# Optimization experiments

Hardware: AMD Instinct MI355X
Metric: run time of the kernel (lower is better)

Reference implementation:

```python
import jax, jax.numpy as jnp
import numpy as np
import math

D_MODEL = 768
NUM_HEADS = 12
HEAD_DIM = D_MODEL // NUM_HEADS
HIDDEN = 3072
EPS = 1e-05
CLAMP = 1e9


def setup_inputs() -> dict:
    key = jax.random.key(0)
    ks = jax.random.split(key, 8)
    s = 0.02
    return {
        "x": jax.random.normal(ks[0], (1, 4096, D_MODEL), dtype=jnp.float32),
        "gamma1": jnp.ones((D_MODEL,), jnp.float32),
        "beta1": jnp.zeros((D_MODEL,), jnp.float32),
        "Wqkv": jax.random.normal(ks[1], (D_MODEL, 3 * D_MODEL), jnp.float32) * s,
        "bqkv": jnp.zeros((3 * D_MODEL,), jnp.float32),
        "Wo": jax.random.normal(ks[2], (D_MODEL, D_MODEL), jnp.float32) * s,
        "bo": jnp.zeros((D_MODEL,), jnp.float32),
        "gamma2": jnp.ones((D_MODEL,), jnp.float32),
        "beta2": jnp.zeros((D_MODEL,), jnp.float32),
        "W1": jax.random.normal(ks[3], (D_MODEL, HIDDEN), jnp.float32) * s,
        "b1": jnp.zeros((HIDDEN,), jnp.float32),
        "W2": jax.random.normal(ks[4], (HIDDEN, D_MODEL), jnp.float32) * s,
        "b2": jnp.zeros((D_MODEL,), jnp.float32),
    }


def layer_norm(x, gamma, beta):
    mean = jnp.mean(x, axis=-1, keepdims=True)
    var = jnp.mean((x - mean) ** 2, axis=-1, keepdims=True)
    y = (x - mean) / jnp.sqrt(var + EPS)
    return gamma * y + beta


def attention_block(x, Wqkv, bqkv, Wo, bo):
    B, S, D = x.shape
    qkv = x @ Wqkv + bqkv                             # [B,S,3D]
    qkv = qkv.reshape(B, S, NUM_HEADS, 3 * HEAD_DIM).transpose(0, 2, 1, 3)  # [B,H,S,3hd]
    q, k, v = jnp.split(qkv, 3, axis=-1)              # each [B,H,S,hd]
    scaled = jnp.einsum("bhqd,bhkd->bhqk", q, k) / math.sqrt(HEAD_DIM)
    causal = jnp.tril(jnp.ones((S, S), dtype=bool))
    scaled = jnp.where(causal, scaled, -jnp.inf)
    scaled = jnp.clip(scaled, -CLAMP, CLAMP)          # torch clamp turns -inf into -1e9
    attn = jax.nn.softmax(scaled, axis=-1)
    vals = jnp.einsum("bhqk,bhkd->bhqd", attn, v)     # [B,H,S,hd]
    vals = vals.transpose(0, 2, 1, 3).reshape(B, S, D)
    return vals @ Wo + bo


def ffn_block(x, W1, b1, W2, b2):
    h = jax.nn.gelu(x @ W1 + b1, approximate=False)
    return h @ W2 + b2


def reference(x, gamma1, beta1, Wqkv, bqkv, Wo, bo, gamma2, beta2, W1, b1, W2, b2):
    x = x + attention_block(layer_norm(x, gamma1, beta1), Wqkv, bqkv, Wo, bo)
    x = x + ffn_block(layer_norm(x, gamma2, beta2), W1, b1, W2, b2)
    return x
```

## Files before the change

### kernel.cpp

```cpp
#include <hip/hip_runtime.h>
#include <hip/hip_bf16.h>
#include <cmath>

using u16 = unsigned short;
typedef __bf16 bf16x8 __attribute__((ext_vector_type(8)));
typedef __bf16 bf16x2 __attribute__((ext_vector_type(2)));
typedef unsigned short u16x8 __attribute__((ext_vector_type(8)));
typedef unsigned short u16x4 __attribute__((ext_vector_type(4)));
typedef float f32x4 __attribute__((ext_vector_type(4)));

#define SEQ 4096
#define DM 768
#define NH 12
#define HD 64
#define HID 3072

#define GLD_LDS16(g, l) __builtin_amdgcn_global_load_lds( \
    (const __attribute__((address_space(1))) void*)(g),   \
    (__attribute__((address_space(3))) void*)(l), 16, 0, 0)

__device__ __forceinline__ u16 f2bf(float f) {
    union { float f; unsigned u; } v; v.f = f;
    unsigned r = v.u + 0x7fffu + ((v.u >> 16) & 1u);
    return (u16)(r >> 16);
}

__device__ __forceinline__ unsigned pack_bf16(float a, float b) {
    union { bf16x2 v; unsigned u; } c;
    c.v[0] = (__bf16)a; c.v[1] = (__bf16)b;
    return c.u;
}

__device__ __forceinline__ float gelu_exact(float v) {
    float z = fabsf(v) * 0.70710678118654752f;
    float t = __builtin_amdgcn_rcpf(__builtin_fmaf(0.3275911f, z, 1.0f));
    float p = t * __builtin_fmaf(t, __builtin_fmaf(t, __builtin_fmaf(t,
                __builtin_fmaf(t, 1.061405429f, -1.453152027f),
                1.421413741f), -0.284496736f), 0.254829592f);
    float e = __builtin_amdgcn_exp2f(-z * z * 1.44269504088896341f);
    float erfv = __builtin_fmaf(-p, e, 1.0f);
    erfv = (v < 0.0f) ? -erfv : erfv;
    return 0.5f * v * (1.0f + erfv);
}

__device__ __forceinline__ int swz64(int row, int k) {
    return (row << 6) | ((((k >> 3) ^ row) & 7) << 3) | (k & 7);
}
__device__ __forceinline__ int swz128(int row, int k) {
    return (row << 7) | ((((k >> 3) ^ row) & 15) << 3) | (k & 7);
}

__device__ __forceinline__ void ln_row(const float* __restrict__ xr,
                                       const float* __restrict__ g,
                                       const float* __restrict__ b,
                                       u16* __restrict__ yr, int t) {
    float v0 = xr[t], v1 = xr[t + 256], v2 = xr[t + 512];
    float s = v0 + v1 + v2;
#pragma unroll
    for (int m = 32; m; m >>= 1) s += __shfl_xor(s, m);
    __shared__ float red[4], red2[4];
    int wid = t >> 6, lane = t & 63;
    if (lane == 0) red[wid] = s;
    __syncthreads();
    float mean = (red[0] + red[1] + red[2] + red[3]) * (1.0f / DM);
    float d0 = v0 - mean, d1 = v1 - mean, d2 = v2 - mean;
    float q = d0 * d0 + d1 * d1 + d2 * d2;
#pragma unroll
    for (int m = 32; m; m >>= 1) q += __shfl_xor(q, m);
    if (lane == 0) red2[wid] = q;
    __syncthreads();
    float var = (red2[0] + red2[1] + red2[2] + red2[3]) * (1.0f / DM);
    float rstd = rsqrtf(var + 1e-5f);
    yr[t]       = f2bf(d0 * rstd * g[t]       + b[t]);
    yr[t + 256] = f2bf(d1 * rstd * g[t + 256] + b[t + 256]);
    yr[t + 512] = f2bf(d2 * rstd * g[t + 512] + b[t + 512]);
}

__global__ __launch_bounds__(256) void prep_kernel(
    const float* __restrict__ x, const float* __restrict__ g1, const float* __restrict__ b1,
    const float* __restrict__ Wqkv, const float* __restrict__ Wo,
    const float* __restrict__ W1, const float* __restrict__ W2,
    u16* __restrict__ WqkvT, u16* __restrict__ WoT,
    u16* __restrict__ W1T, u16* __restrict__ W2T, u16* __restrict__ y) {
    int bid = blockIdx.x;
    if (bid < 6912) {
        const float* W; u16* Wt; int K, N, ntx, b;
        if (bid < 1728)      { W = Wqkv; Wt = WqkvT; K = 768;  N = 2304; ntx = 72; b = bid; }
        else if (bid < 2304) { W = Wo;   Wt = WoT;   K = 768;  N = 768;  ntx = 24; b = bid - 1728; }
        else if (bid < 4608) { W = W1;   Wt = W1T;   K = 768;  N = 3072; ntx = 96; b = bid - 2304; }
        else                 { W = W2;   Wt = W2T;   K = 3072; N = 768;  ntx = 24; b = bid - 4608; }
        int nb = (b % ntx) * 32, kb = (b / ntx) * 32;
        __shared__ float tile[32][33];
        int tx = threadIdx.x & 31, ty = threadIdx.x >> 5;
#pragma unroll
        for (int i = 0; i < 32; i += 8)
            tile[ty + i][tx] = W[(size_t)(kb + ty + i) * N + nb + tx];
        __syncthreads();
#pragma unroll
        for (int i = 0; i < 32; i += 8)
            Wt[(size_t)(nb + ty + i) * K + kb + tx] = f2bf(tile[tx][ty + i]);
    } else {
        int row = bid - 6912;
        ln_row(x + (size_t)row * DM, g1, b1, y + (size_t)row * DM, threadIdx.x);
    }
}

__global__ __launch_bounds__(256) void ln_kernel(const float* __restrict__ x,
                                                 const float* __restrict__ g,
                                                 const float* __restrict__ b,
                                                 u16* __restrict__ y) {
    int row = blockIdx.x;
    ln_row(x + (size_t)row * DM, g, b, y + (size_t)row * DM, threadIdx.x);
}

template<int TM, int TN>
__global__ __launch_bounds__(256) void gemm_bf16(
    const u16* __restrict__ A, const u16* __restrict__ Bt,
    const float* __restrict__ bias, const float* __restrict__ resid,
    float* __restrict__ outF, u16* __restrict__ outB, u16* __restrict__ vtg,
    int M, int N, int K, int gelu) {
    constexpr int APR = TM / 32;
    constexpr int BPR = TN / 32;
    constexpr int GL = APR + BPR;
    constexpr int MF = (TN == 128) ? 4 : 2;
    constexpr int NF = 2;
    __shared__ __align__(16) u16 As[2][TM * 64];
    __shared__ __align__(16) u16 Bs[2][TN * 64];
    int tid = threadIdx.x;
    int lane = tid & 63, wid = tid >> 6;
    int lr = lane & 15, hi = lane >> 4;
    int wrow = (TN == 128) ? 0 : (wid >> 1) * 32;
    int wcol = (TN == 128) ? wid * 32 : (wid & 1) * 32;
    int m0 = blockIdx.y * TM, n0 = blockIdx.x * TN;

    f32x4 acc[MF][NF] = {};
    int rsub = wid * 8 + (lane >> 3);
    int chunk = lane & 7;

    auto STAGE = [&](int buf, int kt) {
#pragma unroll
        for (int p = 0; p < APR; ++p) {
            int row = p * 32 + rsub;
            int col = kt + (((chunk ^ row) & 7) << 3);
            GLD_LDS16(A + (size_t)(m0 + row) * K + col, &As[buf][(p * 32 + wid * 8) * 64]);
        }
#pragma unroll
        for (int p = 0; p < BPR; ++p) {
            int row = p * 32 + rsub;
            int col = kt + (((chunk ^ row) & 7) << 3);
            GLD_LDS16(Bt + (size_t)(n0 + row) * K + col, &Bs[buf][(p * 32 + wid * 8) * 64]);
        }
    };

    int NT = K >> 6;
    STAGE(0, 0);
    STAGE(1, 64);
    for (int t = 0; t < NT; ++t) {
        if (t + 1 < NT) asm volatile("s_waitcnt vmcnt(%0)" :: "i"(GL) : "memory");
        else            asm volatile("s_waitcnt vmcnt(0)" ::: "memory");
        __builtin_amdgcn_s_barrier();
        const u16* as = &As[t & 1][0];
        const u16* bs = &Bs[t & 1][0];
#pragma unroll
        for (int ks = 0; ks < 2; ++ks) {
            bf16x8 af[MF], bfr[NF];
#pragma unroll
            for (int m = 0; m < MF; ++m)
                af[m] = *reinterpret_cast<const bf16x8*>(&as[swz64(wrow + m * 16 + lr, ks * 32 + hi * 8)]);
#pragma unroll
            for (int n = 0; n < NF; ++n)
                bfr[n] = *reinterpret_cast<const bf16x8*>(&bs[swz64(wcol + n * 16 + lr, ks * 32 + hi * 8)]);
            __builtin_amdgcn_s_setprio(1);
#pragma unroll
            for (int m = 0; m < MF; ++m)
#pragma unroll
                for (int n = 0; n < NF; ++n)
                    acc[m][n] = __builtin_amdgcn_mfma_f32_16x16x32_bf16(af[m], bfr[n], acc[m][n], 0, 0, 0);
            __builtin_amdgcn_s_setprio(0);
        }
        __builtin_amdgcn_s_barrier();
        if (t + 2 < NT) STAGE(t & 1, (t + 2) << 6);
    }
#pragma unroll
    for (int m = 0; m < MF; ++m) {
#pragma unroll
        for (int n = 0; n < NF; ++n) {
            int col = n0 + wcol + n * 16 + lr;
            float bv = bias[col];
            u16 q4[4];
#pragma unroll
            for (int r = 0; r < 4; ++r) {
                int row = m0 + wrow + m * 16 + hi * 4 + r;
                float v = acc[m][n][r] + bv;
                if (gelu) v = gelu_exact(v);
                if (resid) v += resid[(size_t)row * N + col];
                q4[r] = f2bf(v);
                if (outF) outF[(size_t)row * N + col] = v;
                if (outB) outB[(size_t)row * N + col] = q4[r];
            }
            if (vtg) {
                int h = col / 192;
                int c = col - h * 192;
                if (c >= 128) {
                    int row0 = m0 + wrow + m * 16 + hi * 4;
                    u16x4 vv; vv[0] = q4[0]; vv[1] = q4[1]; vv[2] = q4[2]; vv[3] = q4[3];
                    *reinterpret_cast<u16x4*>(&vtg[(size_t)(h * 64 + c - 128) * SEQ + row0]) = vv;
                }
            }
        }
    }
}

__global__ __launch_bounds__(256, 2) void attn_kernel(const u16* __restrict__ qkv,
                                                      const u16* __restrict__ VtG,
                                                      u16* __restrict__ attn) {
    __shared__ __align__(16) u16 Ks[2][128 * 64];
    __shared__ __align__(16) u16 Vt[2][64 * 128];
    int tid = threadIdx.x;
    int lane = tid & 63, w = tid >> 6;
    int lr = lane & 15, hi = lane >> 4;
    int upper = hi >> 1;
    const float SCL = 0.125f * 1.44269504088896340736f;

    int bid = blockIdx.x;
    int h = bid % NH;
    int qb = (SEQ / 64 - 1) - bid / NH;

    int qrow = qb * 64 + w * 16 + lr;
    bf16x8 qf[2];
#pragma unroll
    for (int ks = 0; ks < 2; ++ks)
        qf[ks] = *reinterpret_cast<const bf16x8*>(&qkv[(size_t)qrow * 2304 + h * 192 + ks * 32 + hi * 8]);

    f32x4 acc[4] = {};
    float m_run = -INFINITY, l_run = 0.0f;

    int skvr = tid >> 3;
    int skc = (tid & 7) << 3;
    int svd = tid >> 4;
    int svk = (tid & 15) << 3;
    u16x8 kr[4], vr[4];

    auto LOADKV = [&](int kb) {
#pragma unroll
        for (int p = 0; p < 4; ++p)
            kr[p] = *reinterpret_cast<const u16x8*>(
                &qkv[(size_t)(kb * 128 + skvr + p * 32) * 2304 + h * 192 + 64 + skc]);
#pragma unroll
        for (int p = 0; p < 4; ++p)
            vr[p] = *reinterpret_cast<const u16x8*>(
                &VtG[(size_t)(h * 64 + svd + p * 16) * SEQ + kb * 128 + svk]);
    };
    auto WRITEKV = [&](int buf) {
#pragma unroll
        for (int p = 0; p < 4; ++p)
            *reinterpret_cast<u16x8*>(&Ks[buf][swz64(skvr + p * 32, skc)]) = kr[p];
#pragma unroll
        for (int p = 0; p < 4; ++p)
            *reinterpret_cast<u16x8*>(&Vt[buf][swz128(svd + p * 16, svk)]) = vr[p];
    };

    int nt = (qb * 64 + 64 + 127) >> 7;
    LOADKV(0);
    WRITEKV(0);
    for (int kb = 0; kb < nt; ++kb) {
        if (kb + 1 < nt) LOADKV(kb + 1);
        __syncthreads();
        const u16* ksb = &Ks[kb & 1][0];
        const u16* vtb = &Vt[kb & 1][0];

        f32x4 s[8] = {};
        __builtin_amdgcn_s_setprio(1);
#pragma unroll
        for (int ks = 0; ks < 2; ++ks) {
#pragma unroll
            for (int n = 0; n < 8; ++n) {
                bf16x8 kf = *reinterpret_cast<const bf16x8*>(&ksb[swz64(n * 16 + lr, ks * 32 + hi * 8)]);
                s[n] = __builtin_amdgcn_mfma_f32_16x16x32_bf16(kf, qf[ks], s[n], 0, 0, 0);
            }
        }
        __builtin_amdgcn_s_setprio(0);
        float sv[8][4];
#pragma unroll
        for (int n = 0; n < 8; ++n) {
            sv[n][0] = s[n][0]; sv[n][1] = s[n][1]; sv[n][2] = s[n][2]; sv[n][3] = s[n][3];
        }
        if (kb == nt - 1) {
#pragma unroll
            for (int n = 0; n < 8; ++n)
#pragma unroll
                for (int r = 0; r < 4; ++r) {
                    int kv = kb * 128 + n * 16 + hi * 4 + r;
                    if (kv > qrow) sv[n][r] = -3.0e38f;
                }
        }
        float t8[8];
#pragma unroll
        for (int n = 0; n < 8; ++n)
            t8[n] = fmaxf(fmaxf(sv[n][0], sv[n][1]), fmaxf(sv[n][2], sv[n][3]));
        float mx = fmaxf(fmaxf(fmaxf(t8[0], t8[1]), fmaxf(t8[2], t8[3])),
                         fmaxf(fmaxf(t8[4], t8[5]), fmaxf(t8[6], t8[7])));
        mx = fmaxf(mx, __shfl_xor(mx, 16));
        mx = fmaxf(mx, __shfl_xor(mx, 32));
        float mxs = mx * SCL;
        if (!__all(mxs <= m_run + 8.0f)) {
            float mnew = fmaxf(m_run, mxs);
            float alpha = __builtin_amdgcn_exp2f(m_run - mnew);
            l_run *= alpha;
#pragma unroll
            for (int n2 = 0; n2 < 4; ++n2)
#pragma unroll
                for (int r = 0; r < 4; ++r) acc[n2][r] *= alpha;
            m_run = mnew;
        }
        float rs = 0.0f;
#pragma unroll
        for (int n = 0; n < 8; ++n) {
            float p0 = __builtin_amdgcn_exp2f(__builtin_fmaf(sv[n][0], SCL, -m_run));
            float p1 = __builtin_amdgcn_exp2f(__builtin_fmaf(sv[n][1], SCL, -m_run));
            float p2 = __builtin_amdgcn_exp2f(__builtin_fmaf(sv[n][2], SCL, -m_run));
            float p3 = __builtin_amdgcn_exp2f(__builtin_fmaf(sv[n][3], SCL, -m_run));
            sv[n][0] = p0; sv[n][1] = p1; sv[n][2] = p2; sv[n][3] = p3;
            rs += (p0 + p1) + (p2 + p3);
        }
        rs += __shfl_xor(rs, 16);
        rs += __shfl_xor(rs, 32);
        l_run += rs;

        unsigned pk0[8], pk1[8];
#pragma unroll
        for (int n = 0; n < 8; ++n) {
            pk0[n] = pack_bf16(sv[n][0], sv[n][1]);
            pk1[n] = pack_bf16(sv[n][2], sv[n][3]);
        }
        int src0 = lr + ((hi & 1) << 5);
        int src1 = src0 + 16;
#pragma unroll
        for (int ks = 0; ks < 4; ++ks) {
            union { unsigned w4[4]; bf16x8 v; } pf;
            {
                unsigned a0 = __shfl(pk0[2 * ks], src0), b0 = __shfl(pk0[2 * ks + 1], src0);
                unsigned a1 = __shfl(pk1[2 * ks], src0), b1 = __shfl(pk1[2 * ks + 1], src0);
                unsigned a2 = __shfl(pk0[2 * ks], src1), b2 = __shfl(pk0[2 * ks + 1], src1);
                unsigned a3 = __shfl(pk1[2 * ks], src1), b3 = __shfl(pk1[2 * ks + 1], src1);
                pf.w4[0] = upper ? b0 : a0;
                pf.w4[1] = upper ? b1 : a1;
                pf.w4[2] = upper ? b2 : a2;
                pf.w4[3] = upper ? b3 : a3;
            }
            __builtin_amdgcn_s_setprio(1);
#pragma unroll
            for (int n2 = 0; n2 < 4; ++n2) {
                bf16x8 vf = *reinterpret_cast<const bf16x8*>(&vtb[swz128(n2 * 16 + lr, ks * 32 + hi * 8)]);
                acc[n2] = __builtin_amdgcn_mfma_f32_16x16x32_bf16(vf, pf.v, acc[n2], 0, 0, 0);
            }
            __builtin_amdgcn_s_setprio(0);
        }
        if (kb + 1 < nt) WRITEKV((kb + 1) & 1);
    }
    float inv = 1.0f / l_run;
#pragma unroll
    for (int n2 = 0; n2 < 4; ++n2) {
#pragma unroll
        for (int r = 0; r < 4; ++r) {
            int dcol = h * 64 + n2 * 16 + hi * 4 + r;
            attn[(size_t)qrow * DM + dcol] = f2bf(acc[n2][r] * inv);
        }
    }
}

extern "C" void kernel_launch(void* const* d_in, const int* in_sizes, int n_in,
                              void* d_out, int out_size, void* d_ws, size_t ws_size,
                              hipStream_t stream) {
    const float* x      = (const float*)d_in[0];
    const float* gamma1 = (const float*)d_in[1];
    const float* beta1  = (const float*)d_in[2];
    const float* Wqkv   = (const float*)d_in[3];
    const float* bqkv   = (const float*)d_in[4];
    const float* Wo     = (const float*)d_in[5];
    const float* bo     = (const float*)d_in[6];
    const float* gamma2 = (const float*)d_in[7];
    const float* beta2  = (const float*)d_in[8];
    const float* W1     = (const float*)d_in[9];
    const float* b1     = (const float*)d_in[10];
    const float* W2     = (const float*)d_in[11];
    const float* b2     = (const float*)d_in[12];

    char* ws = (char*)d_ws;
    size_t off = 0;
    u16* WqkvT = (u16*)(ws + off); off += (size_t)2304 * 768 * 2;
    u16* WoT   = (u16*)(ws + off); off += (size_t)768 * 768 * 2;
    u16* W1T   = (u16*)(ws + off); off += (size_t)3072 * 768 * 2;
    u16* W2T   = (u16*)(ws + off); off += (size_t)768 * 3072 * 2;
    u16* B1    = (u16*)(ws + off); off += (size_t)SEQ * DM * 2;
    u16* Q     = (u16*)(ws + off); off += (size_t)SEQ * HID * 2;
    float* x1  = (float*)(ws + off); off += (size_t)SEQ * DM * 4;

    u16* VtG = (u16*)x1;

    prep_kernel<<<dim3(11008), 256, 0, stream>>>(x, gamma1, beta1, Wqkv, Wo, W1, W2,
                                                 WqkvT, WoT, W1T, W2T, B1);
    gemm_bf16<64, 128><<<dim3(2304 / 128, SEQ / 64), 256, 0, stream>>>(B1, WqkvT, bqkv, nullptr, nullptr, Q, VtG, SEQ, 2304, 768, 0);
    attn_kernel<<<dim3((SEQ / 64) * NH), 256, 0, stream>>>(Q, VtG, B1);
    gemm_bf16<64, 64><<<dim3(768 / 64, SEQ / 64), 256, 0, stream>>>(B1, WoT, bo, x, x1, nullptr, nullptr, SEQ, 768, 768, 0);
    ln_kernel<<<SEQ, 256, 0, stream>>>(x1, gamma2, beta2, B1);
    gemm_bf16<64, 128><<<dim3(3072 / 128, SEQ / 64), 256, 0, stream>>>(B1, W1T, b1, nullptr, nullptr, Q, nullptr, SEQ, 3072, 768, 1);
    gemm_bf16<64, 64><<<dim3(768 / 64, SEQ / 64), 256, 0, stream>>>(Q, W2T, b2, x1, (float*)d_out, nullptr, nullptr, SEQ, 768, 3072, 0);
}
```

Measured before the change: 206.8 us.

## Read V fragments directly from global memory instead of staging through LDS

The attention kernel no longer stages V^T tiles in shared memory. Each lane loads its V fragments straight from the global transposed V buffer right before the PV MFMAs. This halves LDS use per block, so launch bounds rise to 3 blocks per CU for more occupancy. The cost is that every wave re-reads V from global or L2 with no prefetch, so MFMAs can stall on memory latency and redundant V traffic goes up.

```diff
diff --git a/kernel.cpp b/kernel.cpp
--- a/kernel.cpp
+++ b/kernel.cpp
@@ -45,9 +45,6 @@
 
 __device__ __forceinline__ int swz64(int row, int k) {
     return (row << 6) | ((((k >> 3) ^ row) & 7) << 3) | (k & 7);
-}
-__device__ __forceinline__ int swz128(int row, int k) {
-    return (row << 7) | ((((k >> 3) ^ row) & 15) << 3) | (k & 7);
 }
 
 __device__ __forceinline__ void ln_row(const float* __restrict__ xr,
@@ -211,11 +208,10 @@
     }
 }
 
-__global__ __launch_bounds__(256, 2) void attn_kernel(const u16* __restrict__ qkv,
+__global__ __launch_bounds__(256, 3) void attn_kernel(const u16* __restrict__ qkv,
                                                       const u16* __restrict__ VtG,
                                                       u16* __restrict__ attn) {
     __shared__ __align__(16) u16 Ks[2][128 * 64];
-    __shared__ __align__(16) u16 Vt[2][64 * 128];
     int tid = threadIdx.x;
     int lane = tid & 63, w = tid >> 6;
     int lr = lane & 15, hi = lane >> 4;
@@ -237,37 +233,29 @@
 
     int skvr = tid >> 3;
     int skc = (tid & 7) << 3;
-    int svd = tid >> 4;
-    int svk = (tid & 15) << 3;
-    u16x8 kr[4], vr[4];
-
-    auto LOADKV = [&](int kb) {
+    u16x8 kr[4];
+
+    auto LOADK = [&](int kb) {
 #pragma unroll
         for (int p = 0; p < 4; ++p)
             kr[p] = *reinterpret_cast<const u16x8*>(
                 &qkv[(size_t)(kb * 128 + skvr + p * 32) * 2304 + h * 192 + 64 + skc]);
-#pragma unroll
-        for (int p = 0; p < 4; ++p)
-            vr[p] = *reinterpret_cast<const u16x8*>(
-                &VtG[(size_t)(h * 64 + svd + p * 16) * SEQ + kb * 128 + svk]);
     };
-    auto WRITEKV = [&](int buf) {
+    auto WRITEK = [&](int buf) {
 #pragma unroll
         for (int p = 0; p < 4; ++p)
             *reinterpret_cast<u16x8*>(&Ks[buf][swz64(skvr + p * 32, skc)]) = kr[p];
-#pragma unroll
-        for (int p = 0; p < 4; ++p)
-            *reinterpret_cast<u16x8*>(&Vt[buf][swz128(svd + p * 16, svk)]) = vr[p];
     };
 
+    const u16* vrow = &VtG[(size_t)(h * 64 + lr) * SEQ + hi * 8];
+
     int nt = (qb * 64 + 64 + 127) >> 7;
-    LOADKV(0);
-    WRITEKV(0);
+    LOADK(0);
+    WRITEK(0);
     for (int kb = 0; kb < nt; ++kb) {
-        if (kb + 1 < nt) LOADKV(kb + 1);
+        if (kb + 1 < nt) LOADK(kb + 1);
         __syncthreads();
         const u16* ksb = &Ks[kb & 1][0];
-        const u16* vtb = &Vt[kb & 1][0];
 
         f32x4 s[8] = {};
         __builtin_amdgcn_s_setprio(1);
@@ -335,6 +323,7 @@
         }
         int src0 = lr + ((hi & 1) << 5);
         int src1 = src0 + 16;
+        const u16* vt = vrow + kb * 128;
 #pragma unroll
         for (int ks = 0; ks < 4; ++ks) {
             union { unsigned w4[4]; bf16x8 v; } pf;
@@ -348,15 +337,17 @@
                 pf.w4[2] = upper ? b2 : a2;
                 pf.w4[3] = upper ? b3 : a3;
             }
+            bf16x8 vf[4];
+#pragma unroll
+            for (int n2 = 0; n2 < 4; ++n2)
+                vf[n2] = *reinterpret_cast<const bf16x8*>(vt + (size_t)(n2 * 16) * SEQ + ks * 32);
             __builtin_amdgcn_s_setprio(1);
 #pragma unroll
-            for (int n2 = 0; n2 < 4; ++n2) {
-                bf16x8 vf = *reinterpret_cast<const bf16x8*>(&vtb[swz128(n2 * 16 + lr, ks * 32 + hi * 8)]);
-                acc[n2] = __builtin_amdgcn_mfma_f32_16x16x32_bf16(vf, pf.v, acc[n2], 0, 0, 0);
-            }
+            for (int n2 = 0; n2 < 4; ++n2)
+                acc[n2] = __builtin_amdgcn_mfma_f32_16x16x32_bf16(vf[n2], pf.v, acc[n2], 0, 0, 0);
             __builtin_amdgcn_s_setprio(0);
         }
-        if (kb + 1 < nt) WRITEKV((kb + 1) & 1);
+        if (kb + 1 < nt) WRITEK((kb + 1) & 1);
     }
     float inv = 1.0f / l_run;
 #pragma unroll
```

Result: slower. 271.2 us (+31.2%).
